# Performance work log

Hardware: AMD Instinct MI355X
Metric: run time of the kernel (lower is better)

Reference implementation:

```python
import jax, jax.numpy as jnp
import numpy as np

T, B = 1024, 16384
GAMMA = 0.99


def setup_inputs() -> dict:
    key = jax.random.key(0)
    k1, k2, k3, k4 = jax.random.split(key, 4)
    return {
        "target_value": jax.random.normal(k1, (T, B), dtype=jnp.float32),
        "rewards": jax.random.normal(k2, (T, B), dtype=jnp.float32),
        "target_log_policy": jax.random.normal(k3, (T, B), dtype=jnp.float32),
        "behaviour_log_policy": jax.random.normal(k4, (T, B), dtype=jnp.float32),
        "rho": jnp.float32(1.0),
        "cis": jnp.float32(1.0),
    }


def reference(target_value, rewards, target_log_policy, behaviour_log_policy, rho, cis):
    # truncated importance sampling weights
    is_weights = jnp.exp(target_log_policy - behaviour_log_policy)  # (T, B)
    rhos = jnp.minimum(rho, is_weights)
    ciss = jnp.minimum(cis, is_weights)

    v = target_value            # (T, B)
    v_next = v[1:]              # V(x_{s+1}), (T-1, B)
    # delta_s V = rho_s * (r_s + gamma*V(x_{s+1}) - V(x_s))
    delta = rhos[:-1] * (rewards[:-1] + GAMMA * v_next - v[:-1])
    # affine recurrence: vtrace_s = a_s + b_s * vtrace_{s+1}
    a = v[:-1] + delta - GAMMA * ciss[:-1] * v_next  # (T-1, B)
    b = GAMMA * ciss[:-1]                            # (T-1, B)

    def step(carry, ab):
        a_i, b_i = ab
        vt = a_i + b_i * carry
        return vt, vt

    # vtrace[T-1] = V(x_{T-1}); scan backwards in time
    _, vtrace_head = jax.lax.scan(step, v[-1], (a, b), reverse=True)
    # original returns vtrace[:-1].detach(), rhos.detach()
    return (jax.lax.stop_gradient(vtrace_head), jax.lax.stop_gradient(rhos))
```

## Files before the change

kernel.cpp:

```cpp
#include <hip/hip_runtime.h>

#define T_DIM 1024
#define B_DIM 16384
#define GAMMA 0.99f

constexpr int U = 8;

__global__ __launch_bounds__(64, 1)
void vtrace_scan_kernel(const float* __restrict__ v,
                        const float* __restrict__ rew,
                        const float* __restrict__ tlp,
                        const float* __restrict__ blp,
                        const float* __restrict__ rho_p,
                        const float* __restrict__ cis_p,
                        float* __restrict__ out_v,
                        float* __restrict__ out_rho)
{
    const int c = blockIdx.x * 64 + threadIdx.x;
    const float rho_clip = *rho_p;
    const float cis_clip = *cis_p;

    {
        const int idx = (T_DIM - 1) * B_DIM + c;
        float iw = expf(tlp[idx] - blp[idx]);
        out_rho[idx] = fminf(rho_clip, iw);
    }
    float v_next = v[(T_DIM - 1) * B_DIM + c];
    float carry  = v_next;

    float b0r[U], b0t[U], b0b[U], b0v[U];
    float b1r[U], b1t[U], b1b[U], b1v[U];
    float b2r[U], b2t[U], b2b[U], b2v[U];
    float b3r[U], b3t[U], b3b[U], b3v[U];

    auto load_group = [&](int g, float (&br)[U], float (&bt)[U],
                          float (&bb)[U], float (&bv)[U]) {
        const int base = (T_DIM - 2) - g * U;
#pragma unroll
        for (int u = 0; u < U; ++u) {
            const int idx = (base - u) * B_DIM + c;
            br[u] = rew[idx];
            bt[u] = tlp[idx];
            bb[u] = blp[idx];
            bv[u] = v[idx];
        }
    };

    auto compute_group = [&](int g, float (&br)[U], float (&bt)[U],
                             float (&bb)[U], float (&bv)[U]) {
        const int base = (T_DIM - 2) - g * U;
#pragma unroll
        for (int u = 0; u < U; ++u) {
            const int idx = (base - u) * B_DIM + c;
            const float iw    = expf(bt[u] - bb[u]);
            const float rho_t = fminf(rho_clip, iw);
            const float cis_t = fminf(cis_clip, iw);
            out_rho[idx] = rho_t;
            const float gcis = GAMMA * cis_t;
            const float rest = fmaf(rho_t, fmaf(GAMMA, v_next, br[u]) - bv[u], bv[u])
                               - gcis * v_next;
            const float vt = fmaf(gcis, carry, rest);
            out_v[idx] = vt;
            carry  = vt;
            v_next = bv[u];
        }
    };

    auto load_group_last = [&](float (&br)[U], float (&bt)[U],
                               float (&bb)[U], float (&bv)[U]) {
#pragma unroll
        for (int u = 0; u < 7; ++u) {
            const int idx = (6 - u) * B_DIM + c;
            br[u] = rew[idx];
            bt[u] = tlp[idx];
            bb[u] = blp[idx];
            bv[u] = v[idx];
        }
    };

    auto compute_group_last = [&](float (&br)[U], float (&bt)[U],
                                  float (&bb)[U], float (&bv)[U]) {
#pragma unroll
        for (int u = 0; u < 7; ++u) {
            const int idx = (6 - u) * B_DIM + c;
            const float iw    = expf(bt[u] - bb[u]);
            const float rho_t = fminf(rho_clip, iw);
            const float cis_t = fminf(cis_clip, iw);
            out_rho[idx] = rho_t;
            const float gcis = GAMMA * cis_t;
            const float rest = fmaf(rho_t, fmaf(GAMMA, v_next, br[u]) - bv[u], bv[u])
                               - gcis * v_next;
            const float vt = fmaf(gcis, carry, rest);
            out_v[idx] = vt;
            carry  = vt;
            v_next = bv[u];
        }
    };

    load_group(0, b0r, b0t, b0b, b0v);
    load_group(1, b1r, b1t, b1b, b1v);
    load_group(2, b2r, b2t, b2b, b2v);
    load_group(3, b3r, b3t, b3b, b3v);

    for (int g = 0; g < 120; g += 4) {
        compute_group(g,     b0r, b0t, b0b, b0v);
        load_group(g + 4,    b0r, b0t, b0b, b0v);
        compute_group(g + 1, b1r, b1t, b1b, b1v);
        load_group(g + 5,    b1r, b1t, b1b, b1v);
        compute_group(g + 2, b2r, b2t, b2b, b2v);
        load_group(g + 6,    b2r, b2t, b2b, b2v);
        compute_group(g + 3, b3r, b3t, b3b, b3v);
        load_group(g + 7,    b3r, b3t, b3b, b3v);
    }

    compute_group(120, b0r, b0t, b0b, b0v);
    load_group(124,    b0r, b0t, b0b, b0v);
    compute_group(121, b1r, b1t, b1b, b1v);
    load_group(125,    b1r, b1t, b1b, b1v);
    compute_group(122, b2r, b2t, b2b, b2v);
    load_group(126,    b2r, b2t, b2b, b2v);
    compute_group(123, b3r, b3t, b3b, b3v);
    load_group_last(   b3r, b3t, b3b, b3v);

    compute_group(124, b0r, b0t, b0b, b0v);
    compute_group(125, b1r, b1t, b1b, b1v);
    compute_group(126, b2r, b2t, b2b, b2v);
    compute_group_last(b3r, b3t, b3b, b3v);
}

extern "C" void kernel_launch(void* const* d_in, const int* in_sizes, int n_in,
                              void* d_out, int out_size, void* d_ws, size_t ws_size,
                              hipStream_t stream) {
    const float* v    = (const float*)d_in[0];
    const float* rew  = (const float*)d_in[1];
    const float* tlp  = (const float*)d_in[2];
    const float* blp  = (const float*)d_in[3];
    const float* rho  = (const float*)d_in[4];
    const float* cis  = (const float*)d_in[5];

    float* out_v   = (float*)d_out;
    float* out_rho = (float*)d_out + (size_t)(T_DIM - 1) * B_DIM;

    dim3 grid(B_DIM / 64), block(64);
    vtrace_scan_kernel<<<grid, block, 0, stream>>>(v, rew, tlp, blp, rho, cis,
                                                   out_v, out_rho);
}
```

Baseline: 340.5 us.

## Stream timesteps through LDS ring via global_load_lds with manual vmcnt waits

Replaces the register-buffered 4x8 prefetch groups with a 10-deep LDS ring buffer filled by direct global-to-LDS loads, using hand-placed s_waitcnt vmcnt counts so that several timesteps of loads stay in flight. Stores are emitted as inline-asm global_store_dword with a decrementing offset. The aim is to keep more memory requests in flight per wave, frees registers, and avoids compiler-inserted conservative waits on the serial scan. It relies on exact vmcnt accounting, since stores also count toward vmcnt, and on clamped over-prefetch past row 0, so miscounting could introduce races or stalls.

```diff
diff --git a/kernel.cpp b/kernel.cpp
--- a/kernel.cpp
+++ b/kernel.cpp
@@ -2,130 +2,93 @@
 
 #define T_DIM 1024
 #define B_DIM 16384
+#define ROWB  65536
 #define GAMMA 0.99f
 
-constexpr int U = 8;
+
+#define GL(arr, j, a)                                                      \
+  __builtin_amdgcn_global_load_lds(                                        \
+      (const __attribute__((address_space(1))) void*)((arr) + off_c),      \
+      (__attribute__((address_space(3))) void*)&lds[j][a][0], 4, 0, 0)
+
+#define PREF(j)                                                            \
+  do {                                                                     \
+    const int rp = (rowp >= 0) ? rowp : 0;            \
+    const size_t off_c = (size_t)rp * B_DIM + (size_t)c;                   \
+    GL(rew, j, 0); GL(tlp, j, 1); GL(blp, j, 2); GL(vvp, j, 3);            \
+    --rowp;                                                                \
+  } while (0)
+
+#define BODY(j, KW)                                                        \
+  do {                                                                     \
+    asm volatile("s_waitcnt vmcnt(" #KW ")" ::: "memory");                 \
+    __builtin_amdgcn_sched_barrier(0);                                     \
+    const float brw = lds[j][0][tid];                                      \
+    const float btl = lds[j][1][tid];                                      \
+    const float bbl = lds[j][2][tid];                                      \
+    const float bvv = lds[j][3][tid];                                      \
+    const float iw    = expf(btl - bbl);                                   \
+    const float rho_t = fminf(rho_clip, iw);                               \
+    const float cis_t = fminf(cis_clip, iw);                               \
+    const float gcis  = GAMMA * cis_t;                                     \
+    const float rest  = fmaf(rho_t, fmaf(GAMMA, v_next, brw) - bvv, bvv)   \
+                        - gcis * v_next;                                   \
+    const float vt    = fmaf(gcis, carry, rest);                           \
+    asm volatile("global_store_dword %0, %1, %2"                           \
+                 :: "v"(ofs_s), "v"(rho_t), "s"(orho));                    \
+    asm volatile("global_store_dword %0, %1, %2"                           \
+                 :: "v"(ofs_s), "v"(vt), "s"(ov));                         \
+    carry  = vt;                                                           \
+    v_next = bvv;                                                          \
+    ofs_s -= ROWB;                                                         \
+    asm volatile("s_waitcnt lgkmcnt(0)" ::: "memory");    \
+    __builtin_amdgcn_sched_barrier(0);                                     \
+    PREF(j);                                                               \
+  } while (0)
 
 __global__ __launch_bounds__(64, 1)
-void vtrace_scan_kernel(const float* __restrict__ v,
+void vtrace_scan_kernel(const float* __restrict__ vvp,
                         const float* __restrict__ rew,
                         const float* __restrict__ tlp,
                         const float* __restrict__ blp,
                         const float* __restrict__ rho_p,
                         const float* __restrict__ cis_p,
-                        float* __restrict__ out_v,
-                        float* __restrict__ out_rho)
+                        float* __restrict__ ov,
+                        float* __restrict__ orho)
 {
-    const int c = blockIdx.x * 64 + threadIdx.x;
+    __shared__ float lds[10][4][64];
+    const int tid = threadIdx.x;
+    const int c   = blockIdx.x * 64 + tid;
     const float rho_clip = *rho_p;
     const float cis_clip = *cis_p;
 
     {
-        const int idx = (T_DIM - 1) * B_DIM + c;
-        float iw = expf(tlp[idx] - blp[idx]);
-        out_rho[idx] = fminf(rho_clip, iw);
+        const size_t idx = (size_t)(T_DIM - 1) * B_DIM + c;
+        const float iw = expf(tlp[idx] - blp[idx]);
+        orho[idx] = fminf(rho_clip, iw);
     }
-    float v_next = v[(T_DIM - 1) * B_DIM + c];
+    float v_next = vvp[(size_t)(T_DIM - 1) * B_DIM + c];
     float carry  = v_next;
 
-    float b0r[U], b0t[U], b0b[U], b0v[U];
-    float b1r[U], b1t[U], b1b[U], b1v[U];
-    float b2r[U], b2t[U], b2b[U], b2v[U];
-    float b3r[U], b3t[U], b3b[U], b3v[U];
+    asm volatile("" :: "v"(v_next), "v"(rho_clip), "v"(cis_clip));
+    asm volatile("s_waitcnt vmcnt(0)" ::: "memory");
+    __builtin_amdgcn_sched_barrier(0);
 
-    auto load_group = [&](int g, float (&br)[U], float (&bt)[U],
-                          float (&bb)[U], float (&bv)[U]) {
-        const int base = (T_DIM - 2) - g * U;
-#pragma unroll
-        for (int u = 0; u < U; ++u) {
-            const int idx = (base - u) * B_DIM + c;
-            br[u] = rew[idx];
-            bt[u] = tlp[idx];
-            bb[u] = blp[idx];
-            bv[u] = v[idx];
-        }
-    };
+    int rowp  = T_DIM - 2;
+    int ofs_s = (T_DIM - 2) * ROWB + c * 4;
 
-    auto compute_group = [&](int g, float (&br)[U], float (&bt)[U],
-                             float (&bb)[U], float (&bv)[U]) {
-        const int base = (T_DIM - 2) - g * U;
-#pragma unroll
-        for (int u = 0; u < U; ++u) {
-            const int idx = (base - u) * B_DIM + c;
-            const float iw    = expf(bt[u] - bb[u]);
-            const float rho_t = fminf(rho_clip, iw);
-            const float cis_t = fminf(cis_clip, iw);
-            out_rho[idx] = rho_t;
-            const float gcis = GAMMA * cis_t;
-            const float rest = fmaf(rho_t, fmaf(GAMMA, v_next, br[u]) - bv[u], bv[u])
-                               - gcis * v_next;
-            const float vt = fmaf(gcis, carry, rest);
-            out_v[idx] = vt;
-            carry  = vt;
-            v_next = bv[u];
-        }
-    };
+    PREF(0); PREF(1); PREF(2); PREF(3); PREF(4);
+    PREF(5); PREF(6); PREF(7); PREF(8); PREF(9);
 
-    auto load_group_last = [&](float (&br)[U], float (&bt)[U],
-                               float (&bb)[U], float (&bv)[U]) {
-#pragma unroll
-        for (int u = 0; u < 7; ++u) {
-            const int idx = (6 - u) * B_DIM + c;
-            br[u] = rew[idx];
-            bt[u] = tlp[idx];
-            bb[u] = blp[idx];
-            bv[u] = v[idx];
-        }
-    };
+    BODY(0, 36); BODY(1, 38); BODY(2, 40); BODY(3, 42); BODY(4, 44);
+    BODY(5, 46); BODY(6, 48); BODY(7, 50); BODY(8, 52); BODY(9, 54);
 
-    auto compute_group_last = [&](float (&br)[U], float (&bt)[U],
-                                  float (&bb)[U], float (&bv)[U]) {
-#pragma unroll
-        for (int u = 0; u < 7; ++u) {
-            const int idx = (6 - u) * B_DIM + c;
-            const float iw    = expf(bt[u] - bb[u]);
-            const float rho_t = fminf(rho_clip, iw);
-            const float cis_t = fminf(cis_clip, iw);
-            out_rho[idx] = rho_t;
-            const float gcis = GAMMA * cis_t;
-            const float rest = fmaf(rho_t, fmaf(GAMMA, v_next, br[u]) - bv[u], bv[u])
-                               - gcis * v_next;
-            const float vt = fmaf(gcis, carry, rest);
-            out_v[idx] = vt;
-            carry  = vt;
-            v_next = bv[u];
-        }
-    };
-
-    load_group(0, b0r, b0t, b0b, b0v);
-    load_group(1, b1r, b1t, b1b, b1v);
-    load_group(2, b2r, b2t, b2b, b2v);
-    load_group(3, b3r, b3t, b3b, b3v);
-
-    for (int g = 0; g < 120; g += 4) {
-        compute_group(g,     b0r, b0t, b0b, b0v);
-        load_group(g + 4,    b0r, b0t, b0b, b0v);
-        compute_group(g + 1, b1r, b1t, b1b, b1v);
-        load_group(g + 5,    b1r, b1t, b1b, b1v);
-        compute_group(g + 2, b2r, b2t, b2b, b2v);
-        load_group(g + 6,    b2r, b2t, b2b, b2v);
-        compute_group(g + 3, b3r, b3t, b3b, b3v);
-        load_group(g + 7,    b3r, b3t, b3b, b3v);
+    for (int blk = 0; blk < 101; ++blk) {
+        BODY(0, 54); BODY(1, 54); BODY(2, 54); BODY(3, 54); BODY(4, 54);
+        BODY(5, 54); BODY(6, 54); BODY(7, 54); BODY(8, 54); BODY(9, 54);
     }
 
-    compute_group(120, b0r, b0t, b0b, b0v);
-    load_group(124,    b0r, b0t, b0b, b0v);
-    compute_group(121, b1r, b1t, b1b, b1v);
-    load_group(125,    b1r, b1t, b1b, b1v);
-    compute_group(122, b2r, b2t, b2b, b2v);
-    load_group(126,    b2r, b2t, b2b, b2v);
-    compute_group(123, b3r, b3t, b3b, b3v);
-    load_group_last(   b3r, b3t, b3b, b3v);
-
-    compute_group(124, b0r, b0t, b0b, b0v);
-    compute_group(125, b1r, b1t, b1b, b1v);
-    compute_group(126, b2r, b2t, b2b, b2v);
-    compute_group_last(b3r, b3t, b3b, b3v);
+    BODY(0, 54); BODY(1, 54); BODY(2, 54);
 }
 
 extern "C" void kernel_launch(void* const* d_in, const int* in_sizes, int n_in,
```

After: 337.1 us. About the same (-1.0%).
